# Performance work log

Measured on AMD Instinct MI355X. Metric: run time of the kernel, lower is better.

Reference implementation:

```python
import jax, jax.numpy as jnp
import numpy as np

N, CIN, T, HF, WF = 1, 64, 8, 96, 96
C = 256
H, W = HF // 4, WF // 4
K = 27  # 3 dilations (1,3,5) x 3x3 kernel taps

# kernel-tap offsets, ordered: dilation-major, then row-major 3x3 (matches cat order)
_OFFS = np.array([(oy * d, ox * d) for d in (1, 3, 5) for oy in (-1, 0, 1) for ox in (-1, 0, 1)], dtype=np.float32)


def setup_inputs() -> dict:
    key = jax.random.key(0)
    ks = jax.random.split(key, 6)
    return {
        "input": jax.random.normal(ks[0], (N, CIN, T, HF, WF), jnp.float32),
        "flow": 2.0 * jax.random.normal(ks[1], (N, 2, T, H, W), jnp.float32),
        "w_node": 0.02 * jax.random.normal(ks[2], (C, CIN, 4, 4), jnp.float32),  # Conv3d(64,256,(1,4,4)) with unit time-kernel squeezed
        "b_node": jnp.zeros((C,), jnp.float32),
        "w_up": 0.02 * jax.random.normal(ks[3], (C, 64, 4, 4), jnp.float32),  # ConvTranspose3d(256,64,(1,4,4)) weight [in,out,kh,kw]
        "b_up": jnp.zeros((64,), jnp.float32),
        "w_out": 0.05 * jax.random.normal(ks[4], (64, 64), jnp.float32),  # 1x1x1 Conv3d(64,64)
        "b_out": jnp.zeros((64,), jnp.float32),
        "B": T,
    }


def _deform_sample(node, flow):
    # Deformable neighbor sampling for all 3 dilations at once.
    # node [N,C,T,H,W], flow [N,2,T,H,W] (y,x offsets) -> neighbour [N,C,T,H,W,K]
    n, c, t, h, w = node.shape
    off = jnp.asarray(_OFFS)  # [K,2]
    yy = jnp.arange(h, dtype=node.dtype)[:, None]   # [H,1]
    xx = jnp.arange(w, dtype=node.dtype)[None, :]   # [1,W]
    # sampling positions [N,T,K,H,W]
    py = (yy + off[:, 0][:, None, None]) + flow[:, 0][:, :, None]
    px = (xx + off[:, 1][:, None, None]) + flow[:, 1][:, :, None]
    y0 = jnp.floor(py)
    x0 = jnp.floor(px)
    ty = py - y0
    tx = px - x0
    y0 = y0.astype(jnp.int32)
    x0 = x0.astype(jnp.int32)
    nf = node.transpose(0, 2, 1, 3, 4).reshape(n, t, c, h * w)  # [N,T,C,HW]

    def gather(yi, xi):
        valid = ((yi >= 0) & (yi < h) & (xi >= 0) & (xi < w)).astype(node.dtype)
        idx = jnp.clip(yi, 0, h - 1) * w + jnp.clip(xi, 0, w - 1)  # [N,T,K,H,W]
        idx = jnp.broadcast_to(idx.reshape(n, t, 1, K * h * w), (n, t, c, K * h * w))
        v = jnp.take_along_axis(nf, idx, axis=-1).reshape(n, t, c, K, h, w)
        return v * valid[:, :, None]  # zero-pad outside

    samp = (gather(y0, x0) * ((1 - ty) * (1 - tx))[:, :, None]
            + gather(y0, x0 + 1) * ((1 - ty) * tx)[:, :, None]
            + gather(y0 + 1, x0) * (ty * (1 - tx))[:, :, None]
            + gather(y0 + 1, x0 + 1) * (ty * tx)[:, :, None])  # [N,T,C,K,H,W]
    return samp.transpose(0, 2, 1, 4, 5, 3)  # [N,C,T,H,W,K]


def reference(input, flow, w_node, b_node, w_up, b_up, w_out, b_out, B):
    n, cin, t, hf, wf = input.shape
    h, w = hf // 4, wf // 4
    # layer_node: kernel==stride (1,4,4) conv == non-overlapping 4x4 patch projection
    xr = input.reshape(n, cin, t, h, 4, w, 4)
    node = jnp.einsum('ncthawb,ocab->nothw', xr, w_node) + b_node[None, :, None, None, None]  # [N,C,T,H,W]
    c = node.shape[1]

    neighbour = _deform_sample(node, flow)  # [N,C,T,H,W,27] == cat(dcn1,dcn2,dcn3)

    nhw = n * h * w
    node_b = node.transpose(0, 3, 4, 2, 1).reshape(nhw, t, c)                      # [NHW,B,C]
    nb_a = neighbour.transpose(0, 3, 4, 1, 2, 5).reshape(nhw, c, t * K)            # [NHW,C,B*27]
    A = node_b @ nb_a                                                              # [NHW,B,B*27]
    nb_b = neighbour.transpose(0, 3, 4, 2, 5, 1).reshape(nhw, t * K, c)            # [NHW,B*27,C]
    out = (1.0 / 216.0) * (A @ nb_b)                                               # [NHW,B,C]
    out = out.reshape(n, h, w, t, c).transpose(0, 4, 3, 1, 2)                      # [N,C,T,H,W]

    # layer_out: ConvTranspose (k==stride, pad 0) == per-pixel 4x4 block expansion, then 1x1x1 conv
    up = jnp.einsum('ncthw,coab->nothawb', out, w_up).reshape(n, 64, t, 4 * h, 4 * w)
    up = up + b_up[None, :, None, None, None]
    return jnp.einsum('ncthw,oc->nothw', up, w_out) + b_out[None, :, None, None, None]
```

## Files before the change

kernel.cpp:

```cpp
#include <hip/hip_runtime.h>


typedef unsigned short ushort_t;
typedef ushort_t ushort8 __attribute__((ext_vector_type(8)));
typedef __bf16 bf16x8 __attribute__((ext_vector_type(8)));
typedef __bf16 bf16x2 __attribute__((ext_vector_type(2)));
typedef float f32x4 __attribute__((ext_vector_type(4)));
typedef unsigned int uint4v __attribute__((ext_vector_type(4)));

#define NSTR 264
#define TSTR 34
#define ASTR 40

#define OFF_NH0   0
#define OFF_NH1   16896
#define OFF_NT0   33792
#define OFF_NT1   51200
#define OFF_AS    68608
#define OFF_BASES 69888
#define OFF_WTS   73472
#define ATTN_LDS  77056

__device__ __forceinline__ ushort_t f2bf(float f) {
    __bf16 h = (__bf16)f;
    return __builtin_bit_cast(ushort_t, h);
}
__device__ __forceinline__ float blo(unsigned u) { return __uint_as_float(u << 16); }
__device__ __forceinline__ float bhi(unsigned u) { return __uint_as_float(u & 0xffff0000u); }
__device__ __forceinline__ unsigned pk2(float a, float b) {
    bf16x2 v = { (__bf16)a, (__bf16)b };
    return __builtin_bit_cast(unsigned, v);
}
__device__ __forceinline__ unsigned pk2h(__bf16 a, __bf16 b) {
    bf16x2 v = { a, b };
    return __builtin_bit_cast(unsigned, v);
}
__device__ __forceinline__ void gld_lds16(const void* g, void* l) {
    __builtin_amdgcn_global_load_lds(
        (const __attribute__((address_space(1))) unsigned*)g,
        (__attribute__((address_space(3))) unsigned*)l, 16, 0, 0);
}

__global__ __launch_bounds__(256) void k_prep(
    const float* __restrict__ w_node, const float* __restrict__ w_up,
    const float* __restrict__ w_out, const float* __restrict__ b_up,
    const float* __restrict__ b_out,
    ushort_t* __restrict__ w_node_perm, ushort_t* __restrict__ Wf_perm,
    float* __restrict__ bias_tot)
{
    __shared__ float wout_s[4096];
    int tid = threadIdx.x;
    for (int i = tid; i < 4096; i += 256) wout_s[i] = w_out[i];
    __syncthreads();
    int gid = blockIdx.x * 256 + tid;
    #pragma unroll
    for (int r = 0; r < 4; ++r) {
        int e = gid + r * 65536;
        {
            int k = e & 1023, n = e >> 10;
            w_node_perm[(((k >> 3) << 8) + n) * 8 + (k & 7)] = f2bf(w_node[n * 1024 + k]);
        }
        {
            int n = e & 1023, k = e >> 10;
            int o = n >> 4, ab = n & 15;
            const float* wo = wout_s + o * 64;
            const float* wu = w_up + (k << 10) + ab;
            float s = 0.f;
            #pragma unroll 8
            for (int c = 0; c < 64; ++c) s += wo[c] * wu[c << 4];
            Wf_perm[(((k >> 3) << 10) + n) * 8 + (k & 7)] = f2bf(s);
        }
    }
    if (blockIdx.x == 0 && tid < 64) {
        float s = b_out[tid];
        const float* wo = wout_s + tid * 64;
        #pragma unroll 8
        for (int c = 0; c < 64; ++c) s += wo[c] * b_up[c];
        bias_tot[tid] = s;
    }
}

template<int FINAL>
__global__ __launch_bounds__(256) void k_gemm(
    const float* __restrict__ input, const ushort_t* __restrict__ a_bf,
    const ushort_t* __restrict__ w_perm, const float* __restrict__ bias,
    ushort_t* __restrict__ node_bf, float* __restrict__ dout)
{
    constexpr int KS = FINAL ? 4 : 16;
    constexpr int N  = FINAL ? 1024 : 256;
    constexpr int BN = FINAL ? 128 : 64;
    constexpr int NI = FINAL ? 2 : 1;
    constexpr int RB = BN / 32;
    __shared__ __align__(16) ushort_t A_lds[2][2048];
    __shared__ __align__(16) ushort_t B_lds[2][BN * 64];
    int tid  = threadIdx.x;
    int lane = tid & 63, wid = tid >> 6;
    int g = lane >> 4, r16 = lane & 15;
    int m0 = blockIdx.x * 32, n0 = blockIdx.y * BN;

    const float*   inpA = nullptr;
    const ushort_t* finA = nullptr;
    int ldsA_slot;
    if constexpr (!FINAL) {
        int mA = tid & 31, kcA = tid >> 5;
        int m = m0 + mA;
        int t = m / 576, hw = m % 576, hh = hw / 24, ww = hw % 24;
        inpA = input + (size_t)(kcA >> 1) * 73728 + t * 9216 + hh * 384 + ww * 4 + (kcA & 1) * 192;
        ldsA_slot = (kcA * 32 + mA) * 8;
    } else {
        int m = m0 + (tid >> 3), q = tid & 7;
        finA = a_bf + m * 256 + ((q ^ (m & 7)) * 8);
        ldsA_slot = tid * 8;
    }

    f32x4 acc[2][NI];
    #pragma unroll
    for (int i = 0; i < 2; ++i)
        #pragma unroll
        for (int j = 0; j < NI; ++j) acc[i][j] = (f32x4){0.f, 0.f, 0.f, 0.f};

    float4 fa, fb;
    #pragma unroll
    for (int r = 0; r < RB; ++r) {
        int s = r * 256 + tid;
        int kc = s / BN, n = s % BN;
        gld_lds16(w_perm + (size_t)((kc * N + n0 + n) * 8), &B_lds[0][s * 8]);
    }
    if constexpr (FINAL) {
        gld_lds16(finA, &A_lds[0][ldsA_slot]);
    } else {
        fa = *(const float4*)(inpA);
        fb = *(const float4*)(inpA + 96);
        uint4v p;
        p.x = pk2(fa.x, fa.y); p.y = pk2(fa.z, fa.w);
        p.z = pk2(fb.x, fb.y); p.w = pk2(fb.z, fb.w);
        *(uint4v*)&A_lds[0][ldsA_slot] = p;
    }
    __syncthreads();

    for (int kb = 0; kb < KS; ++kb) {
        int cur = kb & 1, nxt = cur ^ 1;
        bool more = (kb + 1 < KS);
        if (more) {
            #pragma unroll
            for (int r = 0; r < RB; ++r) {
                int s = r * 256 + tid;
                int kc = s / BN, n = s % BN;
                gld_lds16(w_perm + (size_t)((((kb + 1) * 8 + kc) * N + n0 + n) * 8),
                          &B_lds[nxt][s * 8]);
            }
            if constexpr (FINAL) {
                gld_lds16(finA + (kb + 1) * 64, &A_lds[nxt][ldsA_slot]);
            } else {
                fa = *(const float4*)(inpA + (size_t)(kb + 1) * 294912);
                fb = *(const float4*)(inpA + (size_t)(kb + 1) * 294912 + 96);
            }
        }
        bf16x8 af[2][2], bfr[NI][2];
        #pragma unroll
        for (int mi = 0; mi < 2; ++mi)
            #pragma unroll
            for (int ks = 0; ks < 2; ++ks) {
                int idx;
                if constexpr (!FINAL) idx = ((ks * 4 + g) * 32 + mi * 16 + r16) * 8;
                else                  idx = (mi * 16 + r16) * 64 + (((ks * 4 + g) ^ (r16 & 7)) * 8);
                af[mi][ks] = __builtin_bit_cast(bf16x8, *(const ushort8*)&A_lds[cur][idx]);
            }
        #pragma unroll
        for (int ni = 0; ni < NI; ++ni)
            #pragma unroll
            for (int ks = 0; ks < 2; ++ks) {
                int idx = ((ks * 4 + g) * BN + wid * (BN / 4) + ni * 16 + r16) * 8;
                bfr[ni][ks] = __builtin_bit_cast(bf16x8, *(const ushort8*)&B_lds[cur][idx]);
            }
        #pragma unroll
        for (int mi = 0; mi < 2; ++mi)
            #pragma unroll
            for (int ni = 0; ni < NI; ++ni)
                #pragma unroll
                for (int ks = 0; ks < 2; ++ks)
                    acc[mi][ni] = __builtin_amdgcn_mfma_f32_16x16x32_bf16(
                        af[mi][ks], bfr[ni][ks], acc[mi][ni], 0, 0, 0);
        if constexpr (!FINAL) {
            if (more) {
                uint4v p;
                p.x = pk2(fa.x, fa.y); p.y = pk2(fa.z, fa.w);
                p.z = pk2(fb.x, fb.y); p.w = pk2(fb.z, fb.w);
                *(uint4v*)&A_lds[nxt][ldsA_slot] = p;
            }
        }
        __syncthreads();
    }

    if constexpr (!FINAL) {
        int n = n0 + wid * 16 + r16;
        float bv = bias[n];
        #pragma unroll
        for (int mi = 0; mi < 2; ++mi)
            #pragma unroll
            for (int rr = 0; rr < 4; ++rr) {
                int m = m0 + mi * 16 + 4 * g + rr;
                node_bf[(size_t)m * 256 + n] = f2bf(acc[mi][0][rr] + bv);
            }
    } else {
        #pragma unroll
        for (int ni = 0; ni < NI; ++ni) {
            int n = n0 + wid * 32 + ni * 16 + r16;
            int o = n >> 4, aa = (n >> 2) & 3, bb = n & 3;
            float bv = bias[o];
            #pragma unroll
            for (int mi = 0; mi < 2; ++mi)
                #pragma unroll
                for (int rr = 0; rr < 4; ++rr) {
                    int m = m0 + mi * 16 + 4 * g + rr;
                    int t = m / 576, hw = m % 576, hh = hw / 24, ww = hw % 24;
                    dout[((size_t)(o * 8 + t) * 96 + hh * 4 + aa) * 96 + ww * 4 + bb]
                        = acc[mi][ni][rr] + bv;
                }
        }
    }
}

__global__ __launch_bounds__(256) void k_attn(
    const ushort_t* __restrict__ node_bf, const float* __restrict__ flow,
    ushort_t* __restrict__ out_bf)
{
    extern __shared__ char smem[];
    ushort_t* A_s   = (ushort_t*)(smem + OFF_AS);
    int*      bases = (int*)(smem + OFF_BASES);
    float*    wts   = (float*)(smem + OFF_WTS);

    int tid  = threadIdx.x;
    int pos  = blockIdx.x;
    int h    = pos / 24, w = pos % 24;
    int lane = tid & 63, wid = tid >> 6;
    int g    = lane >> 4, r16 = lane & 15;

    if (tid < 224) {
        int j = tid;
        float w00 = 0, w01 = 0, w10 = 0, w11 = 0;
        int b00 = 0, b01 = 0, b10 = 0, b11 = 0;
        if (j < 216) {
            int tt = j / 27, kk = j - tt * 27;
            int d  = 2 * (kk / 9) + 1;
            int oy = (kk / 3) % 3 - 1, ox = kk % 3 - 1;
            float fy = flow[tt * 576 + pos];
            float fx = flow[4608 + tt * 576 + pos];
            float py = (float)(h + oy * d) + fy;
            float px = (float)(w + ox * d) + fx;
            float fy0 = floorf(py), fx0 = floorf(px);
            int y0 = (int)fy0, x0 = (int)fx0;
            float ty = py - fy0, tx = px - fx0;
            int y0c = min(max(y0, 0), 23), y1c = min(max(y0 + 1, 0), 23);
            int x0c = min(max(x0, 0), 23), x1c = min(max(x0 + 1, 0), 23);
            float vy0 = (y0 >= 0 && y0 < 24) ? 1.f : 0.f;
            float vy1 = (y0 >= -1 && y0 < 23) ? 1.f : 0.f;
            float vx0 = (x0 >= 0 && x0 < 24) ? 1.f : 0.f;
            float vx1 = (x0 >= -1 && x0 < 23) ? 1.f : 0.f;
            w00 = (1.f - ty) * (1.f - tx) * vy0 * vx0;
            w01 = (1.f - ty) * tx * vy0 * vx1;
            w10 = ty * (1.f - tx) * vy1 * vx0;
            w11 = ty * tx * vy1 * vx1;
            int base_t = tt * 576 * 256;
            b00 = base_t + (y0c * 24 + x0c) * 256;
            b01 = base_t + (y0c * 24 + x1c) * 256;
            b10 = base_t + (y1c * 24 + x0c) * 256;
            b11 = base_t + (y1c * 24 + x1c) * 256;
        }
        bases[j * 4 + 0] = b00; bases[j * 4 + 1] = b01;
        bases[j * 4 + 2] = b10; bases[j * 4 + 3] = b11;
        wts[j * 4 + 0] = w00; wts[j * 4 + 1] = w01;
        wts[j * 4 + 2] = w10; wts[j * 4 + 3] = w11;
    }
    for (int i = tid; i < 320; i += 256) ((unsigned*)A_s)[i] = 0;

    bf16x8 nbf[8];
    if (wid < 2) {
        int t = r16;
        const ushort_t* src = node_bf + ((size_t)(t & 7) * 576 + pos) * 256 + g * 8;
        ushort8 uz = {};
        #pragma unroll
        for (int s = 0; s < 8; ++s) {
            ushort8 uu = *(const ushort8*)(src + s * 32);
            nbf[s] = __builtin_bit_cast(bf16x8, (t < 8) ? uu : uz);
        }
    }

    f32x4 oacc[4];
    #pragma unroll
    for (int i = 0; i < 4; ++i) oacc[i] = (f32x4){0.f, 0.f, 0.f, 0.f};

    __syncthreads();

    const int jp = tid >> 4;
    const int cb = tid & 15;
    uint4v rg[2][8];

    auto prefetch = [&](int TILE) {
        int jA = TILE * 32 + jp * 2;
        int4 bsA = *(const int4*)&bases[jA * 4];
        int4 bsB = *(const int4*)&bases[jA * 4 + 4];
        #pragma unroll
        for (int q = 0; q < 2; ++q) {
            int c0 = cb * 16 + q * 8;
            rg[q][0] = *(const uint4v*)(node_bf + bsA.x + c0);
            rg[q][1] = *(const uint4v*)(node_bf + bsA.y + c0);
            rg[q][2] = *(const uint4v*)(node_bf + bsA.z + c0);
            rg[q][3] = *(const uint4v*)(node_bf + bsA.w + c0);
            rg[q][4] = *(const uint4v*)(node_bf + bsB.x + c0);
            rg[q][5] = *(const uint4v*)(node_bf + bsB.y + c0);
            rg[q][6] = *(const uint4v*)(node_bf + bsB.z + c0);
            rg[q][7] = *(const uint4v*)(node_bf + bsB.w + c0);
        }
    };
    auto combine = [&](int TILE, ushort_t* nh, ushort_t* nt) {
        int jA = TILE * 32 + jp * 2;
        int jl = jp * 2;
        float4 wA = *(const float4*)&wts[jA * 4];
        float4 wB = *(const float4*)&wts[jA * 4 + 4];
        #pragma unroll
        for (int q = 0; q < 2; ++q) {
            int c0 = cb * 16 + q * 8;
            uint4v outA, outB;
            #pragma unroll
            for (int p = 0; p < 4; ++p) {
                unsigned a0 = rg[q][0][p], a1 = rg[q][1][p], a2 = rg[q][2][p], a3 = rg[q][3][p];
                unsigned b0 = rg[q][4][p], b1 = rg[q][5][p], b2 = rg[q][6][p], b3 = rg[q][7][p];
                float aL = wA.x * blo(a0) + wA.y * blo(a1) + wA.z * blo(a2) + wA.w * blo(a3);
                float aH = wA.x * bhi(a0) + wA.y * bhi(a1) + wA.z * bhi(a2) + wA.w * bhi(a3);
                float bL = wB.x * blo(b0) + wB.y * blo(b1) + wB.z * blo(b2) + wB.w * blo(b3);
                float bH = wB.x * bhi(b0) + wB.y * bhi(b1) + wB.z * bhi(b2) + wB.w * bhi(b3);
                __bf16 cAL = (__bf16)aL, cAH = (__bf16)aH;
                __bf16 cBL = (__bf16)bL, cBH = (__bf16)bH;
                outA[p] = pk2h(cAL, cAH);
                outB[p] = pk2h(cBL, cBH);
                *(unsigned*)(nt + (c0 + 2 * p) * TSTR + jl)     = pk2h(cAL, cBL);
                *(unsigned*)(nt + (c0 + 2 * p + 1) * TSTR + jl) = pk2h(cAH, cBH);
            }
            *(uint4v*)(nh + jl * NSTR + c0)       = outA;
            *(uint4v*)(nh + (jl + 1) * NSTR + c0) = outB;
        }
    };

    prefetch(0);
    combine(0, (ushort_t*)(smem + OFF_NH0), (ushort_t*)(smem + OFF_NT0));
    prefetch(1);
    __syncthreads();

    for (int k = 0; k < 7; ++k) {
        int cur = k & 1;
        ushort_t* nh = (ushort_t*)(smem + (cur ? OFF_NH1 : OFF_NH0));
        ushort_t* nt = (ushort_t*)(smem + (cur ? OFF_NT1 : OFF_NT0));

        if (wid < 2) {
            f32x4 aacc = {0.f, 0.f, 0.f, 0.f};
            int jbase = wid * 16;
            #pragma unroll
            for (int s = 0; s < 8; ++s) {
                const ushort_t* bp = nh + (jbase + r16) * NSTR + s * 32 + g * 8;
                bf16x8 bfrag = __builtin_bit_cast(bf16x8, *(const ushort8*)bp);
                aacc = __builtin_amdgcn_mfma_f32_16x16x32_bf16(nbf[s], bfrag, aacc, 0, 0, 0);
            }
            if (g < 2) {
                #pragma unroll
                for (int rr = 0; rr < 4; ++rr)
                    A_s[(4 * g + rr) * ASTR + jbase + r16] = f2bf(aacc[rr] * (1.f / 216.f));
            }
        }
        __syncthreads();

        {
            bf16x8 afrag = __builtin_bit_cast(bf16x8, *(const ushort8*)(A_s + r16 * ASTR + g * 8));
            #pragma unroll
            for (int i = 0; i < 4; ++i) {
                const ushort_t* tp = nt + (wid * 64 + i * 16 + r16) * TSTR + g * 8;
                uint4v uv;
                uv.x = *(const unsigned*)(tp);
                uv.y = *(const unsigned*)(tp + 2);
                uv.z = *(const unsigned*)(tp + 4);
                uv.w = *(const unsigned*)(tp + 6);
                bf16x8 bfrag = __builtin_bit_cast(bf16x8, uv);
                oacc[i] = __builtin_amdgcn_mfma_f32_16x16x32_bf16(afrag, bfrag, oacc[i], 0, 0, 0);
            }
        }
        if (k < 6) {
            ushort_t* nh2 = (ushort_t*)(smem + (cur ? OFF_NH0 : OFF_NH1));
            ushort_t* nt2 = (ushort_t*)(smem + (cur ? OFF_NT0 : OFF_NT1));
            combine(k + 1, nh2, nt2);
            if (k <= 4) prefetch(k + 2);
        }
        __syncthreads();
    }

    if (g < 2) {
        #pragma unroll
        for (int i = 0; i < 4; ++i) {
            int c = wid * 64 + i * 16 + r16;
            #pragma unroll
            for (int rr = 0; rr < 4; ++rr) {
                int t = 4 * g + rr;
                out_bf[((size_t)t * 576 + pos) * 256 + c] = f2bf(oacc[i][rr]);
            }
        }
    }
}

extern "C" void kernel_launch(void* const* d_in, const int* in_sizes, int n_in,
                              void* d_out, int out_size, void* d_ws, size_t ws_size,
                              hipStream_t stream) {
    (void)in_sizes; (void)n_in; (void)out_size; (void)ws_size;
    const float* input  = (const float*)d_in[0];
    const float* flow   = (const float*)d_in[1];
    const float* w_node = (const float*)d_in[2];
    const float* b_node = (const float*)d_in[3];
    const float* w_up   = (const float*)d_in[4];
    const float* b_up   = (const float*)d_in[5];
    const float* w_out  = (const float*)d_in[6];
    const float* b_out  = (const float*)d_in[7];
    float* dout = (float*)d_out;

    char* wsb = (char*)d_ws;
    ushort_t* node_bf = (ushort_t*)wsb;
    ushort_t* out_bf  = (ushort_t*)(wsb + 2359296);
    ushort_t* w_np    = (ushort_t*)(wsb + 4718592);
    ushort_t* wf_p    = (ushort_t*)(wsb + 5242880);
    float*    bias_t  = (float*)(wsb + 5767168);

    k_prep<<<256, 256, 0, stream>>>(w_node, w_up, w_out, b_up, b_out, w_np, wf_p, bias_t);
    k_gemm<0><<<dim3(144, 4), 256, 0, stream>>>(input, nullptr, w_np, b_node, node_bf, nullptr);
    hipFuncSetAttribute(reinterpret_cast<const void*>(k_attn),
                        hipFuncAttributeMaxDynamicSharedMemorySize, ATTN_LDS);
    k_attn<<<576, 256, ATTN_LDS, stream>>>(node_bf, flow, out_bf);
    k_gemm<1><<<dim3(144, 8), 256, 0, stream>>>(nullptr, out_bf, wf_p, bias_t, nullptr, dout);
}
```

Baseline: 75.32 us.

## Fuse final upsample+projection GEMM into attention kernel epilogue

The separate final GEMM launch goes away. Each attention block now stages its 8x256 output tile in LDS with an XOR swizzle and multiplies it by the fused weight (1024 columns) using MFMA. It writes the 4x4-expanded fp32 output directly. This removes the out_bf round trip through global memory and one kernel launch. The cost is that each of the 576 blocks streams the whole 512KB fused weight from global/L2 with uncoalesced-ish 16-byte loads, and the M dimension is only 8 rows of a 16-row MFMA, so half the MFMA work is wasted.

```diff
diff --git a/kernel.cpp b/kernel.cpp
--- a/kernel.cpp
+++ b/kernel.cpp
@@ -80,17 +80,13 @@
     }
 }
 
-template<int FINAL>
-__global__ __launch_bounds__(256) void k_gemm(
-    const float* __restrict__ input, const ushort_t* __restrict__ a_bf,
-    const ushort_t* __restrict__ w_perm, const float* __restrict__ bias,
-    ushort_t* __restrict__ node_bf, float* __restrict__ dout)
+__global__ __launch_bounds__(256) void k_gemm0(
+    const float* __restrict__ input, const ushort_t* __restrict__ w_perm,
+    const float* __restrict__ bias, ushort_t* __restrict__ node_bf)
 {
-    constexpr int KS = FINAL ? 4 : 16;
-    constexpr int N  = FINAL ? 1024 : 256;
-    constexpr int BN = FINAL ? 128 : 64;
-    constexpr int NI = FINAL ? 2 : 1;
-    constexpr int RB = BN / 32;
+    constexpr int KS = 16;
+    constexpr int N  = 256;
+    constexpr int BN = 64;
     __shared__ __align__(16) ushort_t A_lds[2][2048];
     __shared__ __align__(16) ushort_t B_lds[2][BN * 64];
     int tid  = threadIdx.x;
@@ -98,39 +94,26 @@
     int g = lane >> 4, r16 = lane & 15;
     int m0 = blockIdx.x * 32, n0 = blockIdx.y * BN;
 
-    const float*   inpA = nullptr;
-    const ushort_t* finA = nullptr;
-    int ldsA_slot;
-    if constexpr (!FINAL) {
-        int mA = tid & 31, kcA = tid >> 5;
-        int m = m0 + mA;
-        int t = m / 576, hw = m % 576, hh = hw / 24, ww = hw % 24;
-        inpA = input + (size_t)(kcA >> 1) * 73728 + t * 9216 + hh * 384 + ww * 4 + (kcA & 1) * 192;
-        ldsA_slot = (kcA * 32 + mA) * 8;
-    } else {
-        int m = m0 + (tid >> 3), q = tid & 7;
-        finA = a_bf + m * 256 + ((q ^ (m & 7)) * 8);
-        ldsA_slot = tid * 8;
-    }
-
-    f32x4 acc[2][NI];
-    #pragma unroll
-    for (int i = 0; i < 2; ++i)
-        #pragma unroll
-        for (int j = 0; j < NI; ++j) acc[i][j] = (f32x4){0.f, 0.f, 0.f, 0.f};
+    int mA = tid & 31, kcA = tid >> 5;
+    int m = m0 + mA;
+    int t = m / 576, hw = m % 576, hh = hw / 24, ww = hw % 24;
+    const float* inpA = input + (size_t)(kcA >> 1) * 73728 + t * 9216 + hh * 384 + ww * 4 + (kcA & 1) * 192;
+    int ldsA_slot = (kcA * 32 + mA) * 8;
+
+    f32x4 acc[2];
+    acc[0] = (f32x4){0.f, 0.f, 0.f, 0.f};
+    acc[1] = (f32x4){0.f, 0.f, 0.f, 0.f};
 
     float4 fa, fb;
     #pragma unroll
-    for (int r = 0; r < RB; ++r) {
+    for (int r = 0; r < 2; ++r) {
         int s = r * 256 + tid;
         int kc = s / BN, n = s % BN;
         gld_lds16(w_perm + (size_t)((kc * N + n0 + n) * 8), &B_lds[0][s * 8]);
     }
-    if constexpr (FINAL) {
-        gld_lds16(finA, &A_lds[0][ldsA_slot]);
-    } else {
-        fa = *(const float4*)(inpA);
-        fb = *(const float4*)(inpA + 96);
+    fa = *(const float4*)(inpA);
+    fb = *(const float4*)(inpA + 96);
+    {
         uint4v p;
         p.x = pk2(fa.x, fa.y); p.y = pk2(fa.z, fa.w);
         p.z = pk2(fb.x, fb.y); p.w = pk2(fb.z, fb.w);
@@ -143,87 +126,58 @@
         bool more = (kb + 1 < KS);
         if (more) {
             #pragma unroll
-            for (int r = 0; r < RB; ++r) {
+            for (int r = 0; r < 2; ++r) {
                 int s = r * 256 + tid;
                 int kc = s / BN, n = s % BN;
                 gld_lds16(w_perm + (size_t)((((kb + 1) * 8 + kc) * N + n0 + n) * 8),
                           &B_lds[nxt][s * 8]);
             }
-            if constexpr (FINAL) {
-                gld_lds16(finA + (kb + 1) * 64, &A_lds[nxt][ldsA_slot]);
-            } else {
-                fa = *(const float4*)(inpA + (size_t)(kb + 1) * 294912);
-                fb = *(const float4*)(inpA + (size_t)(kb + 1) * 294912 + 96);
-            }
-        }
-        bf16x8 af[2][2], bfr[NI][2];
+            fa = *(const float4*)(inpA + (size_t)(kb + 1) * 294912);
+            fb = *(const float4*)(inpA + (size_t)(kb + 1) * 294912 + 96);
+        }
+        bf16x8 af[2][2], bfr[2];
         #pragma unroll
         for (int mi = 0; mi < 2; ++mi)
             #pragma unroll
             for (int ks = 0; ks < 2; ++ks) {
-                int idx;
-                if constexpr (!FINAL) idx = ((ks * 4 + g) * 32 + mi * 16 + r16) * 8;
-                else                  idx = (mi * 16 + r16) * 64 + (((ks * 4 + g) ^ (r16 & 7)) * 8);
+                int idx = ((ks * 4 + g) * 32 + mi * 16 + r16) * 8;
                 af[mi][ks] = __builtin_bit_cast(bf16x8, *(const ushort8*)&A_lds[cur][idx]);
             }
         #pragma unroll
-        for (int ni = 0; ni < NI; ++ni)
-            #pragma unroll
-            for (int ks = 0; ks < 2; ++ks) {
-                int idx = ((ks * 4 + g) * BN + wid * (BN / 4) + ni * 16 + r16) * 8;
-                bfr[ni][ks] = __builtin_bit_cast(bf16x8, *(const ushort8*)&B_lds[cur][idx]);
-            }
+        for (int ks = 0; ks < 2; ++ks) {
+            int idx = ((ks * 4 + g) * BN + wid * 16 + r16) * 8;
+            bfr[ks] = __builtin_bit_cast(bf16x8, *(const ushort8*)&B_lds[cur][idx]);
+        }
         #pragma unroll
         for (int mi = 0; mi < 2; ++mi)
             #pragma unroll
-            for (int ni = 0; ni < NI; ++ni)
-                #pragma unroll
-                for (int ks = 0; ks < 2; ++ks)
-                    acc[mi][ni] = __builtin_amdgcn_mfma_f32_16x16x32_bf16(
-                        af[mi][ks], bfr[ni][ks], acc[mi][ni], 0, 0, 0);
-        if constexpr (!FINAL) {
-            if (more) {
-                uint4v p;
-                p.x = pk2(fa.x, fa.y); p.y = pk2(fa.z, fa.w);
-                p.z = pk2(fb.x, fb.y); p.w = pk2(fb.z, fb.w);
-                *(uint4v*)&A_lds[nxt][ldsA_slot] = p;
-            }
+            for (int ks = 0; ks < 2; ++ks)
+                acc[mi] = __builtin_amdgcn_mfma_f32_16x16x32_bf16(
+                    af[mi][ks], bfr[ks], acc[mi], 0, 0, 0);
+        if (more) {
+            uint4v p;
+            p.x = pk2(fa.x, fa.y); p.y = pk2(fa.z, fa.w);
+            p.z = pk2(fb.x, fb.y); p.w = pk2(fb.z, fb.w);
+            *(uint4v*)&A_lds[nxt][ldsA_slot] = p;
         }
         __syncthreads();
     }
 
-    if constexpr (!FINAL) {
-        int n = n0 + wid * 16 + r16;
-        float bv = bias[n];
-        #pragma unroll
-        for (int mi = 0; mi < 2; ++mi)
-            #pragma unroll
-            for (int rr = 0; rr < 4; ++rr) {
-                int m = m0 + mi * 16 + 4 * g + rr;
-                node_bf[(size_t)m * 256 + n] = f2bf(acc[mi][0][rr] + bv);
-            }
-    } else {
-        #pragma unroll
-        for (int ni = 0; ni < NI; ++ni) {
-            int n = n0 + wid * 32 + ni * 16 + r16;
-            int o = n >> 4, aa = (n >> 2) & 3, bb = n & 3;
-            float bv = bias[o];
-            #pragma unroll
-            for (int mi = 0; mi < 2; ++mi)
-                #pragma unroll
-                for (int rr = 0; rr < 4; ++rr) {
-                    int m = m0 + mi * 16 + 4 * g + rr;
-                    int t = m / 576, hw = m % 576, hh = hw / 24, ww = hw % 24;
-                    dout[((size_t)(o * 8 + t) * 96 + hh * 4 + aa) * 96 + ww * 4 + bb]
-                        = acc[mi][ni][rr] + bv;
-                }
-        }
-    }
+    int n = n0 + wid * 16 + r16;
+    float bv = bias[n];
+    #pragma unroll
+    for (int mi = 0; mi < 2; ++mi)
+        #pragma unroll
+        for (int rr = 0; rr < 4; ++rr) {
+            int mm = m0 + mi * 16 + 4 * g + rr;
+            node_bf[(size_t)mm * 256 + n] = f2bf(acc[mi][rr] + bv);
+        }
 }
 
 __global__ __launch_bounds__(256) void k_attn(
     const ushort_t* __restrict__ node_bf, const float* __restrict__ flow,
-    ushort_t* __restrict__ out_bf)
+    const ushort_t* __restrict__ wf_p, const float* __restrict__ bias_t,
+    float* __restrict__ dout)
 {
     extern __shared__ char smem[];
     ushort_t* A_s   = (ushort_t*)(smem + OFF_AS);
@@ -392,6 +346,7 @@
         __syncthreads();
     }
 
+    ushort_t* out_s = (ushort_t*)(smem + OFF_NH1);
     if (g < 2) {
         #pragma unroll
         for (int i = 0; i < 4; ++i) {
@@ -399,7 +354,36 @@
             #pragma unroll
             for (int rr = 0; rr < 4; ++rr) {
                 int t = 4 * g + rr;
-                out_bf[((size_t)t * 576 + pos) * 256 + c] = f2bf(oacc[i][rr]);
+                out_s[t * 256 + (c ^ ((t & 7) << 3))] = f2bf(oacc[i][rr]);
+            }
+        }
+    }
+    __syncthreads();
+
+    bf16x8 af[8];
+    #pragma unroll
+    for (int ks = 0; ks < 8; ++ks) {
+        int e = r16 * 256 + ((ks * 32 + g * 8) ^ ((r16 & 7) << 3));
+        af[ks] = __builtin_bit_cast(bf16x8, *(const ushort8*)(out_s + e));
+    }
+
+    int aa = r16 >> 2, bb = r16 & 3;
+    #pragma unroll 2
+    for (int nf = 0; nf < 16; ++nf) {
+        f32x4 bacc = {0.f, 0.f, 0.f, 0.f};
+        const ushort_t* wp = wf_p + (size_t)(wid * 256 + nf * 16 + r16) * 8 + (size_t)g * 8192;
+        #pragma unroll
+        for (int ks = 0; ks < 8; ++ks) {
+            bf16x8 bfr = __builtin_bit_cast(bf16x8, *(const ushort8*)(wp + (size_t)ks * 32768));
+            bacc = __builtin_amdgcn_mfma_f32_16x16x32_bf16(af[ks], bfr, bacc, 0, 0, 0);
+        }
+        if (g < 2) {
+            int o = wid * 16 + nf;
+            float bv = bias_t[o];
+            #pragma unroll
+            for (int rr = 0; rr < 4; ++rr) {
+                int t = 4 * g + rr;
+                dout[((size_t)(o * 8 + t) * 96 + h * 4 + aa) * 96 + w * 4 + bb] = bacc[rr] + bv;
             }
         }
     }
@@ -421,15 +405,13 @@
 
     char* wsb = (char*)d_ws;
     ushort_t* node_bf = (ushort_t*)wsb;
-    ushort_t* out_bf  = (ushort_t*)(wsb + 2359296);
-    ushort_t* w_np    = (ushort_t*)(wsb + 4718592);
-    ushort_t* wf_p    = (ushort_t*)(wsb + 5242880);
-    float*    bias_t  = (float*)(wsb + 5767168);
+    ushort_t* w_np    = (ushort_t*)(wsb + 2359296);
+    ushort_t* wf_p    = (ushort_t*)(wsb + 2883584);
+    float*    bias_t  = (float*)(wsb + 3407872);
 
     k_prep<<<256, 256, 0, stream>>>(w_node, w_up, w_out, b_up, b_out, w_np, wf_p, bias_t);
-    k_gemm<0><<<dim3(144, 4), 256, 0, stream>>>(input, nullptr, w_np, b_node, node_bf, nullptr);
+    k_gemm0<<<dim3(144, 4), 256, 0, stream>>>(input, w_np, b_node, node_bf);
     hipFuncSetAttribute(reinterpret_cast<const void*>(k_attn),
                         hipFuncAttributeMaxDynamicSharedMemorySize, ATTN_LDS);
-    k_attn<<<576, 256, ATTN_LDS, stream>>>(node_bf, flow, out_bf);
-    k_gemm<1><<<dim3(144, 8), 256, 0, stream>>>(nullptr, out_bf, wf_p, bias_t, nullptr, dout);
-}
+    k_attn<<<576, 256, ATTN_LDS, stream>>>(node_bf, flow, wf_p, bias_t, dout);
+}
```

After: 107.9 us. 1.43x slower.
